# Kernel optimization log

Hardware: AMD Instinct MI355X
Metric: run time of the kernel (lower is better)

## Reference

```python
import jax, jax.numpy as jnp
import numpy as np

B, N, E = 32, 196, 512      # batch, image regions, encoder_dim
D, EMB, V = 512, 512, 32000  # decoder_dim, embedding_dim, vocab
MAXLEN = 65


def setup_inputs() -> dict:
    key = jax.random.key(0)
    ks = jax.random.split(key, 16)
    s = lambda *sh: 1.0 / np.sqrt(sh[-1])
    return {
        "image_features": jax.random.normal(ks[0], (B, N, E), jnp.float32),
        "captions": jax.random.randint(ks[1], (B, MAXLEN), 0, V),
        "emb": jax.random.normal(ks[2], (V, EMB), jnp.float32) * 0.02,
        "Wh0": jax.random.normal(ks[3], (D, E), jnp.float32) * s(E),
        "bh0": jnp.zeros((D,), jnp.float32),
        "Wc0": jax.random.normal(ks[4], (D, E), jnp.float32) * s(E),
        "bc0": jnp.zeros((D,), jnp.float32),
        "Wenc": jax.random.normal(ks[5], (D, E), jnp.float32) * s(E),
        "Wdec": jax.random.normal(ks[6], (D, D), jnp.float32) * s(D),
        "v_att": jax.random.normal(ks[7], (D,), jnp.float32) * s(D),
        "W_ih": jax.random.normal(ks[8], (4 * D, EMB + E), jnp.float32) * s(EMB + E),
        "b_ih": jnp.zeros((4 * D,), jnp.float32),
        "W_hh": jax.random.normal(ks[9], (4 * D, D), jnp.float32) * s(D),
        "b_hh": jnp.zeros((4 * D,), jnp.float32),
        "Wfc": jax.random.normal(ks[10], (V, D), jnp.float32) * s(D),
        "bfc": jnp.zeros((V,), jnp.float32),
    }


def reference(image_features, captions, emb, Wh0, bh0, Wc0, bc0,
              Wenc, Wdec, v_att, W_ih, b_ih, W_hh, b_hh, Wfc, bfc):
    seq_len = captions.shape[1] - 1
    emb_caps = emb[captions]                     # [B, maxlen, EMB]
    xs = jnp.swapaxes(emb_caps[:, :seq_len], 0, 1)  # [T, B, EMB]

    feat_mean = image_features.mean(axis=1)      # [B, E]
    h0 = feat_mean @ Wh0.T + bh0                 # [B, D]
    c0 = feat_mean @ Wc0.T + bc0
    feat_proj = jnp.einsum('bne,de->bnd', image_features, Wenc)  # [B, N, D]

    def step(carry, xt):
        h, c = carry
        # Bahdanau additive attention over the N image regions
        e = jnp.einsum('bnd,d->bn', jnp.tanh(feat_proj + (h @ Wdec.T)[:, None, :]), v_att)
        alpha = jax.nn.softmax(e, axis=-1)                       # [B, N]
        ctx = jnp.einsum('bn,bne->be', alpha, image_features)    # [B, E]
        x = jnp.concatenate([xt, ctx], axis=-1)                  # [B, EMB+E]
        gates = x @ W_ih.T + b_ih + h @ W_hh.T + b_hh            # [B, 4D]
        i, f, g, o = jnp.split(gates, 4, axis=-1)
        c_new = jax.nn.sigmoid(f) * c + jax.nn.sigmoid(i) * jnp.tanh(g)
        h_new = jax.nn.sigmoid(o) * jnp.tanh(c_new)
        out = h_new @ Wfc.T + bfc                                # [B, V]
        return (h_new, c_new), (out, alpha)
    # dropout_p=0.0 -> dropout is identity (eval-mode reference)
    _, (outs, alphas) = jax.lax.scan(step, (h0, c0), xs)
    outputs = jnp.swapaxes(outs, 0, 1)            # [B, T, V]
    attention_weights = jnp.swapaxes(alphas, 0, 1)  # [B, T, N]
    return outputs, attention_weights
```

## Files before the change

kernel.cpp:

```cpp
#include <hip/hip_runtime.h>
#include <cstdint>
#include <cstddef>

typedef _Float16 half2_t __attribute__((ext_vector_type(2)));
typedef _Float16 half4_t __attribute__((ext_vector_type(4)));
typedef _Float16 half8_t __attribute__((ext_vector_type(8)));
typedef float    float4_t __attribute__((ext_vector_type(4)));

#define CAPLEN 65
#define PTLD 200

#define AT_LD(p)     __hip_atomic_load((p), __ATOMIC_RELAXED, __HIP_MEMORY_SCOPE_AGENT)
#define AT_ST(p, v)  __hip_atomic_store((p), (v), __ATOMIC_RELAXED, __HIP_MEMORY_SCOPE_AGENT)

#if defined(__has_builtin)
#if __has_builtin(__builtin_amdgcn_fdot2)
#define HAS_FDOT2 1
#endif
#endif

__device__ __forceinline__ float fdot2f(half2_t a, half2_t b, float c) {
#ifdef HAS_FDOT2
  return __builtin_amdgcn_fdot2(a, b, c, false);
#else
  return c + (float)a[0]*(float)b[0] + (float)a[1]*(float)b[1];
#endif
}

__device__ __forceinline__ float fast_tanh(float x) {
  float e = __expf(2.f*x);
  return 1.f - 2.f/(e + 1.f);
}
__device__ __forceinline__ float fast_sig(float x) {
  return 1.f/(1.f + __expf(-x));
}

__global__ void cvt_k(const float* __restrict__ s, _Float16* __restrict__ d, int n) {
  int i = (blockIdx.x*blockDim.x + threadIdx.x)*4;
  if (i < n) {
    float4 v = *(const float4*)(s + i);
    half4_t h;
    h[0] = (_Float16)v.x; h[1] = (_Float16)v.y; h[2] = (_Float16)v.z; h[3] = (_Float16)v.w;
    *(half4_t*)(d + i) = h;
  }
}

__global__ void bias_sum_k(const float* __restrict__ a, const float* __restrict__ b,
                           float* __restrict__ o, unsigned* __restrict__ bar) {
  int i = blockIdx.x*blockDim.x + threadIdx.x;
  if (i < 2048) o[i] = a[i] + b[i];
  if (i < 1024) bar[i] = 0u;
}

__global__ void gather_emb_k(const float* __restrict__ emb, const int* __restrict__ cap,
                             _Float16* __restrict__ X) {
  int r = blockIdx.x;
  int t = r >> 5, b = r & 31;
  int tok = cap[b*CAPLEN + t];
  const float* s = emb + (size_t)tok*512;
  _Float16* d = X + (size_t)r*512;
  for (int k = threadIdx.x; k < 512; k += blockDim.x) d[k] = (_Float16)s[k];
}

__global__ void init_state_k(const float* __restrict__ imgf,
                             const float* __restrict__ Wh0, const float* __restrict__ bh0,
                             const float* __restrict__ Wc0, const float* __restrict__ bc0,
                             float* __restrict__ c_state, unsigned* __restrict__ hpub2) {
  __shared__ float fm[512];
  __shared__ float hsh[512];
  int b = blockIdx.x, tid = threadIdx.x;
  for (int dI = tid; dI < 512; dI += 256) {
    float s = 0.f;
    const float* p = imgf + ((size_t)b*196)*512 + dI;
    for (int n = 0; n < 196; n++) s += p[(size_t)n*512];
    fm[dI] = s * (1.f/196.f);
  }
  __syncthreads();
  for (int dI = tid; dI < 512; dI += 256) {
    const float* wh = Wh0 + (size_t)dI*512;
    const float* wc = Wc0 + (size_t)dI*512;
    float h = bh0[dI], c = bc0[dI];
    for (int k = 0; k < 512; k++) { h += fm[k]*wh[k]; c += fm[k]*wc[k]; }
    hsh[dI] = h;
    c_state[b*512 + dI] = c;
  }
  __syncthreads();
  {
    half2_t h2; h2[0] = (_Float16)hsh[2*tid]; h2[1] = (_Float16)hsh[2*tid+1];
    union { half2_t h; unsigned u; } cv; cv.h = h2;
    hpub2[b*256 + tid] = cv.u;
  }
}

template<int MODE>
__global__ void __launch_bounds__(256) gemm_abt_k(const _Float16* __restrict__ A, int lda,
    const _Float16* __restrict__ B, int ldb, void* __restrict__ Cp, int ldc,
    const float* __restrict__ bias, int K) {
  int wave = threadIdx.x >> 6, lane = threadIdx.x & 63;
  int m0 = blockIdx.y*128 + (wave >> 1)*64;
  int n0 = blockIdx.x*128 + (wave & 1)*64;
  int lr = lane & 15, quad = lane >> 4;
  float4_t acc[4][4];
  #pragma unroll
  for (int i = 0; i < 4; i++)
    #pragma unroll
    for (int j = 0; j < 4; j++)
      acc[i][j] = (float4_t){0.f, 0.f, 0.f, 0.f};
  const _Float16* Ap = A + (size_t)(m0 + lr)*lda + quad*8;
  const _Float16* Bp = B + (size_t)(n0 + lr)*ldb + quad*8;
  for (int k0 = 0; k0 < K; k0 += 32) {
    half8_t af[4], bf[4];
    #pragma unroll
    for (int i = 0; i < 4; i++) af[i] = *(const half8_t*)(Ap + (size_t)i*16*lda + k0);
    #pragma unroll
    for (int i = 0; i < 4; i++) bf[i] = *(const half8_t*)(Bp + (size_t)i*16*ldb + k0);
    #pragma unroll
    for (int mi = 0; mi < 4; mi++)
      #pragma unroll
      for (int ni = 0; ni < 4; ni++)
        acc[mi][ni] = __builtin_amdgcn_mfma_f32_16x16x32_f16(af[mi], bf[ni], acc[mi][ni], 0, 0, 0);
  }
  #pragma unroll
  for (int mi = 0; mi < 4; mi++) {
    #pragma unroll
    for (int ni = 0; ni < 4; ni++) {
      int col = n0 + ni*16 + lr;
      float bv = (MODE == 1) ? 0.f : bias[col];
      #pragma unroll
      for (int r = 0; r < 4; r++) {
        int row = m0 + mi*16 + quad*4 + r;
        if (MODE == 1) {
          ((_Float16*)Cp)[(size_t)row*ldc + col] = (_Float16)acc[mi][ni][r];
        } else {
          ((float*)Cp)[(size_t)row*ldc + col] = acc[mi][ni][r] + bv;
        }
      }
    }
  }
}

__global__ void __launch_bounds__(256) gemm_pt_k(const _Float16* __restrict__ A, int lda,
    const _Float16* __restrict__ Bimg, _Float16* __restrict__ Cpt, int mrows) {
  int z = blockIdx.z;
  const _Float16* B = Bimg + (size_t)z*196*512;
  _Float16* C = Cpt + (size_t)z*mrows*PTLD;
  int wave = threadIdx.x >> 6, lane = threadIdx.x & 63;
  int m0 = blockIdx.y*128 + (wave >> 1)*64;
  int n0 = blockIdx.x*128 + (wave & 1)*64;
  int lr = lane & 15, quad = lane >> 4;
  float4_t acc[4][4];
  #pragma unroll
  for (int i = 0; i < 4; i++)
    #pragma unroll
    for (int j = 0; j < 4; j++)
      acc[i][j] = (float4_t){0.f, 0.f, 0.f, 0.f};
  const _Float16* Ap = A + (size_t)(m0 + lr)*lda + quad*8;
  const _Float16* Bp = B + (size_t)(n0 + lr)*512 + quad*8;
  for (int k0 = 0; k0 < 512; k0 += 32) {
    half8_t af[4], bf[4];
    #pragma unroll
    for (int i = 0; i < 4; i++) af[i] = *(const half8_t*)(Ap + (size_t)i*16*lda + k0);
    #pragma unroll
    for (int i = 0; i < 4; i++) bf[i] = *(const half8_t*)(Bp + (size_t)i*16*512 + k0);
    #pragma unroll
    for (int mi = 0; mi < 4; mi++)
      #pragma unroll
      for (int ni = 0; ni < 4; ni++)
        acc[mi][ni] = __builtin_amdgcn_mfma_f32_16x16x32_f16(af[mi], bf[ni], acc[mi][ni], 0, 0, 0);
  }
  #pragma unroll
  for (int mi = 0; mi < 4; mi++) {
    #pragma unroll
    for (int ni = 0; ni < 4; ni++) {
      int col = n0 + ni*16 + lr;
      if (col < PTLD) {
        #pragma unroll
        for (int r = 0; r < 4; r++) {
          int row = m0 + mi*16 + quad*4 + r;
          C[(size_t)row*PTLD + col] = (_Float16)acc[mi][ni][r];
        }
      }
    }
  }
}

__device__ __forceinline__ void sbar(unsigned* __restrict__ slots, int r,
                                     unsigned target, int tid) {
  __syncthreads();
  if (tid == 0) AT_ST(slots + r, target);
  if (tid < 8) {
    while (AT_LD(slots + tid) < target) __builtin_amdgcn_s_sleep(1);
  }
  __syncthreads();
}

__global__ void __launch_bounds__(512) loop_k(
    const _Float16* __restrict__ Wdec_h,
    const _Float16* __restrict__ Whh_h,
    const _Float16* __restrict__ fproj_T,
    const _Float16* __restrict__ P_T,
    const float*    __restrict__ Xg,
    const float*    __restrict__ v_att,
    const float*    __restrict__ c_init,
    unsigned*       __restrict__ hpub2,
    float*          __restrict__ epub,
    _Float16*       __restrict__ H_h,
    float*          __restrict__ out_alpha,
    unsigned*       __restrict__ bar) {
  __shared__ _Float16 P_lds[98*256*2];
  __shared__ _Float16 fp_lds[64*PTLD];
  __shared__ __align__(16) unsigned hl_u[256];
  __shared__ float vlf[64];
  __shared__ float hwf[64];
  __shared__ float ep[2][256];
  __shared__ float redA[8];
  __shared__ float redB[8];
  __shared__ float sa[256];
  __shared__ float sm2[512];
  __shared__ float hnl[64];
  int bid = blockIdx.x, tid = threadIdx.x;
  int r = bid & 7, b = bid >> 3;
  unsigned* slots = bar + b*32;
  int row = tid & 255, half = tid >> 8;
  int typ = row >> 6, dl = row & 63;
  int grow = typ*512 + r*64 + dl;
  int lane = tid & 63;

  if (tid < 64) vlf[tid] = v_att[r*64 + tid];
  float c_reg = (tid < 64) ? c_init[b*512 + r*64 + tid] : 0.f;

  if (tid < 256) {
    const _Float16* pp = P_T + ((size_t)b*2048 + grow)*PTLD;
    half2_t* P2 = (half2_t*)P_lds;
    for (int k8 = 0; k8 < 24; k8++) {
      half8_t v8 = *(const half8_t*)(pp + k8*8);
      #pragma unroll
      for (int j2 = 0; j2 < 4; j2++) {
        half2_t h2; h2[0] = v8[2*j2]; h2[1] = v8[2*j2+1];
        P2[(k8*4 + j2)*256 + row] = h2;
      }
    }
    half4_t v4 = *(const half4_t*)(pp + 192);
    half2_t a2; a2[0] = v4[0]; a2[1] = v4[1];
    half2_t b2; b2[0] = v4[2]; b2[1] = v4[3];
    P2[96*256 + row] = a2;
    P2[97*256 + row] = b2;
  } else {
    for (int i = tid - 256; i < 64*25; i += 256) {
      int d = i/25, c = i - d*25;
      *(half8_t*)(fp_lds + d*PTLD + c*8) =
        *(const half8_t*)(fproj_T + ((size_t)(b*512 + r*64 + d))*PTLD + c*8);
    }
  }
  int eBase = (r < 4) ? r*25 : 100 + (r-4)*24;
  int eCnt  = (r < 4) ? 25 : 24;

  for (int t = 0; t < 64; ++t) {
    if (tid < 256) hl_u[tid] = AT_LD(hpub2 + b*256 + tid);
    float xg = (half == 0) ? Xg[((size_t)t*32 + b)*2048 + grow] : 0.f;
    __syncthreads();
    {
      int dim = tid >> 3, s = tid & 7;
      const half8_t* wr = (const half8_t*)(Wdec_h + (size_t)(r*64 + dim)*512 + s*64);
      const half8_t* hh = ((const half8_t*)(const _Float16*)hl_u) + s*8;
      float a = 0.f;
      #pragma unroll
      for (int k8 = 0; k8 < 8; k8++) {
        half8_t w8 = wr[k8]; half8_t h8 = hh[k8];
        const half2_t* wp = (const half2_t*)&w8;
        const half2_t* hp = (const half2_t*)&h8;
        a = fdot2f(wp[0], hp[0], a);
        a = fdot2f(wp[1], hp[1], a);
        a = fdot2f(wp[2], hp[2], a);
        a = fdot2f(wp[3], hp[3], a);
      }
      a += __shfl_xor(a, 1);
      a += __shfl_xor(a, 2);
      a += __shfl_xor(a, 4);
      if (s == 0) hwf[dim] = a;
    }
    __syncthreads();
    {
      float a = 0.f;
      if (row < 196) {
        #pragma unroll 8
        for (int j = 0; j < 32; j++) {
          int dd = half*32 + j;
          a += vlf[dd] * fast_tanh((float)fp_lds[dd*PTLD + row] + hwf[dd]);
        }
      }
      ep[half][row] = a;
    }
    __syncthreads();
    if (tid < 196) AT_ST(epub + ((size_t)b*8 + r)*256 + tid, ep[0][tid] + ep[1][tid]);
    float gacc = xg;
    {
      const half8_t* wr = (const half8_t*)(Whh_h + (size_t)grow*512 + half*256);
      const half8_t* hh = ((const half8_t*)(const _Float16*)hl_u) + half*32;
      for (int k8 = 0; k8 < 32; k8++) {
        half8_t w8 = wr[k8]; half8_t h8 = hh[k8];
        const half2_t* wp = (const half2_t*)&w8;
        const half2_t* hp = (const half2_t*)&h8;
        gacc = fdot2f(wp[0], hp[0], gacc);
        gacc = fdot2f(wp[1], hp[1], gacc);
        gacc = fdot2f(wp[2], hp[2], gacc);
        gacc = fdot2f(wp[3], hp[3], gacc);
      }
    }
    sbar(slots, r, 2*(unsigned)t + 1, tid);

    float ee = -1e30f;
    if (tid < 196) {
      float s0 = 0.f;
      #pragma unroll
      for (int rr = 0; rr < 8; rr++)
        s0 += AT_LD(epub + ((size_t)b*8 + rr)*256 + tid);
      ee = s0;
    }
    {
      float m = ee;
      #pragma unroll
      for (int off = 32; off > 0; off >>= 1) m = fmaxf(m, __shfl_xor(m, off));
      if (lane == 0) redA[tid >> 6] = m;
    }
    __syncthreads();
    float mx = redA[0];
    #pragma unroll
    for (int i = 1; i < 8; i++) mx = fmaxf(mx, redA[i]);
    float ex = (tid < 196) ? __expf(ee - mx) : 0.f;
    {
      float s = ex;
      #pragma unroll
      for (int off = 32; off > 0; off >>= 1) s += __shfl_xor(s, off);
      if (lane == 0) redB[tid >> 6] = s;
    }
    __syncthreads();
    float tot = redB[0];
    #pragma unroll
    for (int i = 1; i < 8; i++) tot += redB[i];
    float al = ex * (1.f/tot);
    if (tid < 256) sa[tid] = al;
    if (tid >= eBase && tid < eBase + eCnt)
      out_alpha[((size_t)b*64 + t)*196 + tid] = al;
    __syncthreads();
    {
      const half2_t* P2 = (const half2_t*)P_lds;
      const float2*  sap = (const float2*)sa;
      int n2b = half*49;
      #pragma unroll 7
      for (int n2 = n2b; n2 < n2b + 49; n2++) {
        half2_t p = P2[n2*256 + row];
        float2 s2 = sap[n2];
        gacc += s2.x*(float)p[0] + s2.y*(float)p[1];
      }
      sm2[tid] = gacc;
    }
    __syncthreads();
    if (tid < 64) {
      float ig = sm2[tid]       + sm2[tid + 256];
      float fg = sm2[64 + tid]  + sm2[tid + 320];
      float gg = sm2[128 + tid] + sm2[tid + 384];
      float og = sm2[192 + tid] + sm2[tid + 448];
      float cn = fast_sig(fg)*c_reg + fast_sig(ig)*fast_tanh(gg);
      float hn = fast_sig(og)*fast_tanh(cn);
      c_reg = cn;
      hnl[tid] = hn;
      H_h[((size_t)t*32 + b)*512 + r*64 + tid] = (_Float16)hn;
    }
    __syncthreads();
    if (tid < 32) {
      half2_t h2; h2[0] = (_Float16)hnl[2*tid]; h2[1] = (_Float16)hnl[2*tid+1];
      union { half2_t h; unsigned u; } cv; cv.h = h2;
      AT_ST(hpub2 + b*256 + r*32 + tid, cv.u);
    }
    sbar(slots, r, 2*(unsigned)t + 2, tid);
  }
}

__global__ void __launch_bounds__(512) logits_k(const _Float16* __restrict__ A,
    const _Float16* __restrict__ Bw, float* __restrict__ C,
    const float* __restrict__ bias) {
  int wave = threadIdx.x >> 6, lane = threadIdx.x & 63;
  int lr = lane & 15, quad = lane >> 4;
  int waveM = wave >> 1, waveN = wave & 1;
  int n0 = blockIdx.x*128 + waveN*64;
  const _Float16* Bp = Bw + (size_t)(n0 + lr)*512 + quad*8;
  float bv[4];
  #pragma unroll
  for (int ni = 0; ni < 4; ni++) bv[ni] = bias[n0 + ni*16 + lr];
  for (int it = 0; it < 4; ++it) {
    int m0 = (blockIdx.y*16 + it*4 + waveM)*64;
    const _Float16* Ap = A + (size_t)(m0 + lr)*512 + quad*8;
    float4_t acc[4][4];
    #pragma unroll
    for (int i = 0; i < 4; i++)
      #pragma unroll
      for (int j = 0; j < 4; j++)
        acc[i][j] = (float4_t){0.f, 0.f, 0.f, 0.f};
    for (int k0 = 0; k0 < 512; k0 += 32) {
      half8_t af[4], bf[4];
      #pragma unroll
      for (int i = 0; i < 4; i++) af[i] = *(const half8_t*)(Ap + (size_t)i*16*512 + k0);
      #pragma unroll
      for (int i = 0; i < 4; i++) bf[i] = *(const half8_t*)(Bp + (size_t)i*16*512 + k0);
      #pragma unroll
      for (int mi = 0; mi < 4; mi++)
        #pragma unroll
        for (int ni = 0; ni < 4; ni++)
          acc[mi][ni] = __builtin_amdgcn_mfma_f32_16x16x32_f16(af[mi], bf[ni], acc[mi][ni], 0, 0, 0);
    }
    #pragma unroll
    for (int mi = 0; mi < 4; mi++) {
      #pragma unroll
      for (int ni = 0; ni < 4; ni++) {
        int col = n0 + ni*16 + lr;
        #pragma unroll
        for (int r = 0; r < 4; r++) {
          int row = m0 + mi*16 + quad*4 + r;
          size_t orow = (size_t)((row & 31)*64 + (row >> 5));
          __builtin_nontemporal_store(acc[mi][ni][r] + bv[ni], C + orow*32000 + col);
        }
      }
    }
  }
}

extern "C" void kernel_launch(void* const* d_in, const int* in_sizes, int n_in,
                              void* d_out, int out_size, void* d_ws, size_t ws_size,
                              hipStream_t stream) {
  const float* imgf  = (const float*)d_in[0];
  const int*   cap   = (const int*)d_in[1];
  const float* emb   = (const float*)d_in[2];
  const float* Wh0   = (const float*)d_in[3];
  const float* bh0   = (const float*)d_in[4];
  const float* Wc0   = (const float*)d_in[5];
  const float* bc0   = (const float*)d_in[6];
  const float* Wenc  = (const float*)d_in[7];
  const float* Wdec  = (const float*)d_in[8];
  const float* v_att = (const float*)d_in[9];
  const float* W_ih  = (const float*)d_in[10];
  const float* b_ih  = (const float*)d_in[11];
  const float* W_hh  = (const float*)d_in[12];
  const float* b_hh  = (const float*)d_in[13];
  const float* Wfc   = (const float*)d_in[14];
  const float* bfc   = (const float*)d_in[15];
  float* out = (float*)d_out;
  (void)in_sizes; (void)n_in; (void)out_size; (void)ws_size;

  char* ws = (char*)d_ws;
  size_t off = 0;
  auto alloc = [&](size_t bytes) -> void* {
    void* p = ws + off;
    off += (bytes + 255) & ~(size_t)255;
    return p;
  };
  _Float16* Wenc_h  = (_Float16*)alloc((size_t)512*512*2);
  _Float16* Wdec_h  = (_Float16*)alloc((size_t)512*512*2);
  _Float16* Wih_h   = (_Float16*)alloc((size_t)2048*1024*2);
  _Float16* Whh_h   = (_Float16*)alloc((size_t)2048*512*2);
  _Float16* Wfc_h   = (_Float16*)alloc((size_t)32000*512*2);
  _Float16* imgf_h  = (_Float16*)alloc((size_t)32*196*512*2);
  _Float16* fproj_T = (_Float16*)alloc((size_t)32*512*PTLD*2);
  _Float16* P_T     = (_Float16*)alloc((size_t)32*2048*PTLD*2);
  _Float16* X_h     = (_Float16*)alloc((size_t)64*32*512*2);
  float*    Xg      = (float*)alloc((size_t)64*32*2048*4);
  float*    bsum    = (float*)alloc((size_t)2048*4);
  float*    c_state = (float*)alloc((size_t)32*512*4);
  unsigned* hpub2   = (unsigned*)alloc((size_t)32*256*4);
  float*    epub    = (float*)alloc((size_t)32*8*256*4);
  _Float16* H_h     = (_Float16*)alloc((size_t)2048*512*2);
  unsigned* bar     = (unsigned*)alloc((size_t)4096);

  auto cvt = [&](const float* s, _Float16* d, int n) {
    cvt_k<<<dim3((n/4 + 255)/256), dim3(256), 0, stream>>>(s, d, n);
  };
  cvt(Wenc, Wenc_h, 512*512);
  cvt(Wdec, Wdec_h, 512*512);
  cvt(W_ih, Wih_h, 2048*1024);
  cvt(W_hh, Whh_h, 2048*512);
  cvt(Wfc,  Wfc_h, 32000*512);
  cvt(imgf, imgf_h, 32*196*512);
  bias_sum_k<<<dim3(8), dim3(256), 0, stream>>>(b_ih, b_hh, bsum, bar);
  gather_emb_k<<<dim3(2048), dim3(256), 0, stream>>>(emb, cap, X_h);
  init_state_k<<<dim3(32), dim3(256), 0, stream>>>(imgf, Wh0, bh0, Wc0, bc0, c_state, hpub2);
  gemm_pt_k<<<dim3(2, 4, 32), dim3(256), 0, stream>>>(Wenc_h, 512, imgf_h, fproj_T, 512);
  gemm_pt_k<<<dim3(2, 16, 32), dim3(256), 0, stream>>>(Wih_h + 512, 1024, imgf_h, P_T, 2048);
  gemm_abt_k<0><<<dim3(16, 16), dim3(256), 0, stream>>>(X_h, 512, Wih_h, 1024, Xg, 2048, bsum, 512);

  float* out_alpha = out + (size_t)32*64*32000;
  loop_k<<<dim3(256), dim3(512), 0, stream>>>(Wdec_h, Whh_h, fproj_T, P_T, Xg,
      v_att, c_state, hpub2, epub, H_h, out_alpha, bar);
  logits_k<<<dim3(250, 2), dim3(512), 0, stream>>>(H_h, Wfc_h, out, bfc);
}
```

Measured before the change: 2.093 ms.

## Split barrier into arrive/wait, pad barrier slots, buffer per-step outputs in LDS

Each recurrent-loop barrier is split into arrive and wait phases, so the W_hh gate dot product runs between publishing the attention partial scores and waiting for the other blocks. Barrier slots are padded to a 32-word stride so each block's flag sits on its own cache line and polling does not contend. The per-step H and alpha global stores are buffered in LDS and written once after the loop, taking them off the serial critical path. The cost is extra shared memory and a longer barrier allocation. The Xg load also moves to the other half of the threads.

```diff
diff --git a/kernel.cpp b/kernel.cpp
--- a/kernel.cpp
+++ b/kernel.cpp
@@ -9,6 +9,7 @@
 
 #define CAPLEN 65
 #define PTLD 200
+#define BARSTRIDE 32
 
 #define AT_LD(p)     __hip_atomic_load((p), __ATOMIC_RELAXED, __HIP_MEMORY_SCOPE_AGENT)
 #define AT_ST(p, v)  __hip_atomic_store((p), (v), __ATOMIC_RELAXED, __HIP_MEMORY_SCOPE_AGENT)
@@ -49,7 +50,7 @@
                            float* __restrict__ o, unsigned* __restrict__ bar) {
   int i = blockIdx.x*blockDim.x + threadIdx.x;
   if (i < 2048) o[i] = a[i] + b[i];
-  if (i < 1024) bar[i] = 0u;
+  for (int j = i; j < 32*8*BARSTRIDE; j += 2048) bar[j] = 0u;
 }
 
 __global__ void gather_emb_k(const float* __restrict__ emb, const int* __restrict__ cap,
@@ -184,12 +185,15 @@
   }
 }
 
-__device__ __forceinline__ void sbar(unsigned* __restrict__ slots, int r,
-                                     unsigned target, int tid) {
+__device__ __forceinline__ void sbar_arrive(unsigned* __restrict__ slots, int r,
+                                            unsigned target, int tid) {
   __syncthreads();
-  if (tid == 0) AT_ST(slots + r, target);
+  if (tid == 0) AT_ST(slots + r*BARSTRIDE, target);
+}
+__device__ __forceinline__ void sbar_wait(unsigned* __restrict__ slots,
+                                          unsigned target, int tid) {
   if (tid < 8) {
-    while (AT_LD(slots + tid) < target) __builtin_amdgcn_s_sleep(1);
+    while (AT_LD(slots + tid*BARSTRIDE) < target) __builtin_amdgcn_s_sleep(1);
   }
   __syncthreads();
 }
@@ -210,6 +214,8 @@
   __shared__ _Float16 P_lds[98*256*2];
   __shared__ _Float16 fp_lds[64*PTLD];
   __shared__ __align__(16) unsigned hl_u[256];
+  __shared__ _Float16 Hbuf[64*64];
+  __shared__ float abuf[25*64];
   __shared__ float vlf[64];
   __shared__ float hwf[64];
   __shared__ float ep[2][256];
@@ -220,7 +226,7 @@
   __shared__ float hnl[64];
   int bid = blockIdx.x, tid = threadIdx.x;
   int r = bid & 7, b = bid >> 3;
-  unsigned* slots = bar + b*32;
+  unsigned* slots = bar + b*8*BARSTRIDE;
   int row = tid & 255, half = tid >> 8;
   int typ = row >> 6, dl = row & 63;
   int grow = typ*512 + r*64 + dl;
@@ -257,7 +263,7 @@
 
   for (int t = 0; t < 64; ++t) {
     if (tid < 256) hl_u[tid] = AT_LD(hpub2 + b*256 + tid);
-    float xg = (half == 0) ? Xg[((size_t)t*32 + b)*2048 + grow] : 0.f;
+    float xg = (half == 1) ? Xg[((size_t)t*32 + b)*2048 + grow] : 0.f;
     __syncthreads();
     {
       int dim = tid >> 3, s = tid & 7;
@@ -293,6 +299,7 @@
     }
     __syncthreads();
     if (tid < 196) AT_ST(epub + ((size_t)b*8 + r)*256 + tid, ep[0][tid] + ep[1][tid]);
+    sbar_arrive(slots, r, 2*(unsigned)t + 1, tid);
     float gacc = xg;
     {
       const half8_t* wr = (const half8_t*)(Whh_h + (size_t)grow*512 + half*256);
@@ -307,7 +314,7 @@
         gacc = fdot2f(wp[3], hp[3], gacc);
       }
     }
-    sbar(slots, r, 2*(unsigned)t + 1, tid);
+    sbar_wait(slots, 2*(unsigned)t + 1, tid);
 
     float ee = -1e30f;
     if (tid < 196) {
@@ -341,7 +348,7 @@
     float al = ex * (1.f/tot);
     if (tid < 256) sa[tid] = al;
     if (tid >= eBase && tid < eBase + eCnt)
-      out_alpha[((size_t)b*64 + t)*196 + tid] = al;
+      abuf[(tid - eBase)*64 + t] = al;
     __syncthreads();
     {
       const half2_t* P2 = (const half2_t*)P_lds;
@@ -365,7 +372,7 @@
       float hn = fast_sig(og)*fast_tanh(cn);
       c_reg = cn;
       hnl[tid] = hn;
-      H_h[((size_t)t*32 + b)*512 + r*64 + tid] = (_Float16)hn;
+      Hbuf[t*64 + tid] = (_Float16)hn;
     }
     __syncthreads();
     if (tid < 32) {
@@ -373,7 +380,17 @@
       union { half2_t h; unsigned u; } cv; cv.h = h2;
       AT_ST(hpub2 + b*256 + r*32 + tid, cv.u);
     }
-    sbar(slots, r, 2*(unsigned)t + 2, tid);
+    sbar_arrive(slots, r, 2*(unsigned)t + 2, tid);
+    sbar_wait(slots, 2*(unsigned)t + 2, tid);
+  }
+
+  for (int i = tid; i < 64*64; i += 512) {
+    int t = i >> 6, d = i & 63;
+    H_h[((size_t)t*32 + b)*512 + r*64 + d] = Hbuf[i];
+  }
+  for (int i = tid; i < eCnt*64; i += 512) {
+    int ln = i >> 6, t = i & 63;
+    out_alpha[((size_t)b*64 + t)*196 + eBase + ln] = abuf[ln*64 + t];
   }
 }
 
@@ -469,7 +486,7 @@
   unsigned* hpub2   = (unsigned*)alloc((size_t)32*256*4);
   float*    epub    = (float*)alloc((size_t)32*8*256*4);
   _Float16* H_h     = (_Float16*)alloc((size_t)2048*512*2);
-  unsigned* bar     = (unsigned*)alloc((size_t)4096);
+  unsigned* bar     = (unsigned*)alloc((size_t)32*8*BARSTRIDE*4);
 
   auto cvt = [&](const float* s, _Float16* d, int n) {
     cvt_k<<<dim3((n/4 + 255)/256), dim3(256), 0, stream>>>(s, d, n);
```

Result: faster. 2.027 ms (-3.1%).
